# Optimization experiments

Measured on AMD Instinct MI355X. Metric: run time of the kernel, lower is better.

Reference implementation:

```python
import jax, jax.numpy as jnp
import numpy as np

HIDDEN = 1024
HEADS = 16
HEAD_DIM = HIDDEN // HEADS


def setup_inputs() -> dict:
    key = jax.random.key(0)
    ks = jax.random.split(key, 9)
    B, S, D = 8, 1370, HIDDEN
    x = jax.random.normal(ks[0], (B, S, D), dtype=jnp.float32)
    s = 1.0 / np.sqrt(D)
    Wq = jax.random.normal(ks[1], (D, D), dtype=jnp.float32) * s
    bq = jnp.zeros((D,), dtype=jnp.float32)
    Wk = jax.random.normal(ks[2], (D, D), dtype=jnp.float32) * s
    bk = jnp.zeros((D,), dtype=jnp.float32)
    Wv = jax.random.normal(ks[3], (D, D), dtype=jnp.float32) * s
    bv = jnp.zeros((D,), dtype=jnp.float32)
    Wo = jax.random.normal(ks[4], (D, D), dtype=jnp.float32) * s
    bo = jnp.zeros((D,), dtype=jnp.float32)
    return {"x": x, "Wq": Wq, "bq": bq, "Wk": Wk, "bk": bk,
            "Wv": Wv, "bv": bv, "Wo": Wo, "bo": bo}


def reference(x, Wq, bq, Wk, bk, Wv, bv, Wo, bo):
    B, S, D = x.shape
    H, Dh = HEADS, HEAD_DIM
    # separate Q/K/V projections
    q = (x @ Wq + bq).reshape(B, S, H, Dh).transpose(0, 2, 1, 3)  # [B,H,S,Dh]
    k = (x @ Wk + bk).reshape(B, S, H, Dh).transpose(0, 2, 1, 3)
    v = (x @ Wv + bv).reshape(B, S, H, Dh).transpose(0, 2, 1, 3)
    scale = jnp.asarray(Dh, q.dtype) ** -0.5
    attn = jnp.einsum('bhqd,bhkd->bhqk', q, k) * scale  # [B,H,S,S]
    attn = jax.nn.softmax(attn, axis=-1)
    out = jnp.einsum('bhqk,bhkd->bhqd', attn, v)        # [B,H,S,Dh]
    out = out.transpose(0, 2, 1, 3).reshape(B, S, D)
    return out @ Wo + bo
```

## Files before the change

kernel.cpp:

```cpp
#include <hip/hip_runtime.h>
#include <stdint.h>

#define DEV __device__ __forceinline__

typedef unsigned short u16;
typedef __attribute__((ext_vector_type(8))) __bf16 bf16x8;
typedef __attribute__((ext_vector_type(8))) u16 u16x8;
typedef __attribute__((ext_vector_type(4))) u16 u16x4;
typedef __attribute__((ext_vector_type(4))) float floatx4;

#define S_LEN 1370
#define S_PAD 1408
#define NH 16
#define DH 64
#define M_TOK (8 * S_LEN)
#define NKT (S_PAD / 64)

DEV u16 f2bf(float f) {
    union { float f; uint32_t u; } v; v.f = f;
    uint32_t u = v.u + 0x7fffu + ((v.u >> 16) & 1u);
    return (u16)(u >> 16);
}

typedef const __attribute__((address_space(1))) void as1_cvoid;
typedef __attribute__((address_space(3))) void as3_void;

DEV void async16(const void* g, void* s) {
    __builtin_amdgcn_global_load_lds((as1_cvoid*)g, (as3_void*)s, 16, 0, 0);
}

__global__ void cvt_bf16(const float* __restrict__ src, u16* __restrict__ dst) {
    const size_t i0 = ((size_t)blockIdx.x * 256 + threadIdx.x) * 8;
    const float4 a = *(const float4*)(src + i0);
    const float4 b = *(const float4*)(src + i0 + 4);
    u16x8 o;
    o[0] = f2bf(a.x); o[1] = f2bf(a.y); o[2] = f2bf(a.z); o[3] = f2bf(a.w);
    o[4] = f2bf(b.x); o[5] = f2bf(b.y); o[6] = f2bf(b.z); o[7] = f2bf(b.w);
    *(u16x8*)(dst + i0) = o;
}

__global__ void transpose4(const float* __restrict__ w0, const float* __restrict__ w1,
                           const float* __restrict__ w2, const float* __restrict__ w3,
                           u16* __restrict__ t0, u16* __restrict__ t1,
                           u16* __restrict__ t2, u16* __restrict__ t3) {
    __shared__ u16 tile[64][65];
    const float* src; u16* dst;
    switch (blockIdx.z) {
        case 0: src = w0; dst = t0; break;
        case 1: src = w1; dst = t1; break;
        case 2: src = w2; dst = t2; break;
        default: src = w3; dst = t3; break;
    }
    const int tx = blockIdx.x, ty = blockIdx.y, tid = threadIdx.x;
#pragma unroll
    for (int i = 0; i < 16; i++) {
        int e = i * 256 + tid, r = e >> 6, c = e & 63;
        tile[r][c] = f2bf(src[(size_t)(ty * 64 + r) * 1024 + tx * 64 + c]);
    }
    __syncthreads();
#pragma unroll
    for (int i = 0; i < 16; i++) {
        int e = i * 256 + tid, r = e >> 6, c = e & 63;
        dst[(size_t)(tx * 64 + r) * 1024 + ty * 64 + c] = tile[c][r];
    }
}

template <int MODE>
__global__ void gemm_bt(const u16* __restrict__ A, const u16* __restrict__ BT,
                        const float* __restrict__ bias, void* __restrict__ Cv,
                        int M, int N) {
    __shared__ u16 As[128 * 32];
    __shared__ u16 Bs[128 * 32];
    const int tid = threadIdx.x;
    const int w = tid >> 6, lane = tid & 63, quad = lane >> 4, l15 = lane & 15;
    const int mbase = blockIdx.x * 128, nbase = blockIdx.y * 128;
    const int wm = (w >> 1) * 64, wn = (w & 1) * 64;

    floatx4 acc[4][4];
#pragma unroll
    for (int i = 0; i < 4; i++)
#pragma unroll
        for (int j = 0; j < 4; j++) acc[i][j] = (floatx4){0.f, 0.f, 0.f, 0.f};

    const int srow = tid >> 2;
    const int kb = (tid & 3) * 16;
    int ar0 = mbase + srow;          if (ar0 > M - 1) ar0 = M - 1;
    int ar1 = mbase + 64 + srow;     if (ar1 > M - 1) ar1 = M - 1;
    int br0 = nbase + srow;          if (br0 > N - 1) br0 = N - 1;
    int br1 = nbase + 64 + srow;     if (br1 > N - 1) br1 = N - 1;
    const char* pA = (const char*)A;
    const char* pB = (const char*)BT;
    char* ldsA = (char*)As + w * 1024;
    char* ldsB = (char*)Bs + w * 1024;

    for (int kt = 0; kt < 32; kt++) {
        const int koff = kt * 64 + kb;
        async16(pA + (size_t)ar0 * 2048 + koff, ldsA);
        async16(pA + (size_t)ar1 * 2048 + koff, ldsA + 4096);
        async16(pB + (size_t)br0 * 2048 + koff, ldsB);
        async16(pB + (size_t)br1 * 2048 + koff, ldsB + 4096);
        __syncthreads();
        bf16x8 af[4], bfv[4];
#pragma unroll
        for (int mi = 0; mi < 4; mi++)
            af[mi] = __builtin_bit_cast(bf16x8,
                *(const u16x8*)&As[(wm + mi * 16 + l15) * 32 + quad * 8]);
#pragma unroll
        for (int ni = 0; ni < 4; ni++)
            bfv[ni] = __builtin_bit_cast(bf16x8,
                *(const u16x8*)&Bs[(wn + ni * 16 + l15) * 32 + quad * 8]);
#pragma unroll
        for (int mi = 0; mi < 4; mi++)
#pragma unroll
            for (int ni = 0; ni < 4; ni++)
                acc[mi][ni] = __builtin_amdgcn_mfma_f32_16x16x32_bf16(
                    af[mi], bfv[ni], acc[mi][ni], 0, 0, 0);
        __syncthreads();
    }

    if (MODE == 0 || MODE == 2) {
#pragma unroll
        for (int ni = 0; ni < 4; ni++) {
            const int n = nbase + wn + ni * 16 + l15;
            const float bv = bias[n];
#pragma unroll
            for (int mi = 0; mi < 4; mi++)
#pragma unroll
                for (int r = 0; r < 4; r++) {
                    const int m = mbase + wm + mi * 16 + quad * 4 + r;
                    if (m < M) {
                        if (MODE == 0)
                            ((u16*)Cv)[(size_t)m * 1024 + n] = f2bf(acc[mi][ni][r] + bv);
                        else
                            ((float*)Cv)[(size_t)m * 1024 + n] = acc[mi][ni][r] + bv;
                    }
                }
        }
    } else {
        u16* C = (u16*)Cv;
#pragma unroll
        for (int mi = 0; mi < 4; mi++)
#pragma unroll
            for (int r = 0; r < 4; r++) {
                const int mf = mbase + wm + mi * 16 + quad * 4 + r;
                const int h = mf >> 6, d = mf & 63;
                const float bv = bias[mf];
#pragma unroll
                for (int ni = 0; ni < 4; ni++) {
                    const int t = nbase + wn + ni * 16 + l15;
                    if (t < N) {
                        const int b = t / S_LEN;
                        const int s = t - b * S_LEN;
                        C[(size_t)((b * NH + h) * DH + d) * S_PAD + s] =
                            f2bf(acc[mi][ni][r] + bv);
                    }
                }
            }
    }
}

__global__ void flash_attn(const u16* __restrict__ Q, const u16* __restrict__ K,
                           const u16* __restrict__ VT, u16* __restrict__ O) {
    __shared__ u16 Ks[2 * 64 * 32];
    __shared__ u16 Vs[2 * 64 * 32];
    __shared__ u16 Ps[2][32 * 72];

    const int tid = threadIdx.x;
    const int w = tid >> 6, lane = tid & 63, quad = lane >> 4, l15 = lane & 15;
    const int qt = blockIdx.x, bh = blockIdx.y, b = bh >> 4, h = bh & 15;
    const int q0 = qt * 64 + w * 32;

    bf16x8 qf[2][2];
#pragma unroll
    for (int mi = 0; mi < 2; mi++) {
        int qr = q0 + mi * 16 + l15;
        if (qr > S_LEN - 1) qr = S_LEN - 1;
        const u16* qp = Q + (size_t)(b * S_LEN + qr) * 1024 + h * 64 + quad * 8;
        qf[mi][0] = __builtin_bit_cast(bf16x8, *(const u16x8*)qp);
        qf[mi][1] = __builtin_bit_cast(bf16x8, *(const u16x8*)(qp + 32));
    }

    floatx4 o_acc[2][4];
#pragma unroll
    for (int mi = 0; mi < 2; mi++)
#pragma unroll
        for (int nd = 0; nd < 4; nd++) o_acc[mi][nd] = (floatx4){0.f, 0.f, 0.f, 0.f};
    float mrun[2] = {-1e30f, -1e30f}, lrun[2] = {0.f, 0.f};

    const int scol = ((lane & 3) ^ ((lane >> 3) & 3)) * 16;
    const int lrow = lane >> 2;
    const char* Kbl = (const char*)K + ((size_t)b * S_LEN * 1024 + h * 64) * 2 + scol;
    const char* Vbl = (const char*)VT +
                      ((size_t)(bh * 64 + w * 32 + lrow) * S_PAD) * 2 + scol;
    char* KsB = (char*)Ks;
    char* VsB = (char*)Vs;
    u16* Pw = Ps[w];

    const int rcol = ((quad ^ ((l15 >> 1) & 3)) * 16);

    const float CEXP = 0.18033688f;

    for (int kt = 0; kt < NKT; kt++) {
#pragma unroll
        for (int i = 0; i < 2; i++) {
            const int r0 = w * 32 + i * 16;
            int key = kt * 64 + r0 + lrow;
            if (key > S_LEN - 1) key = S_LEN - 1;
            const char* kg = Kbl + (size_t)key * 2048;
            async16(kg, KsB + r0 * 64);
            async16(kg + 64, KsB + 4096 + r0 * 64);
            const char* vg = Vbl + (size_t)i * (16 * S_PAD * 2) + kt * 128;
            async16(vg, VsB + r0 * 64);
            async16(vg + 64, VsB + 4096 + r0 * 64);
        }
        __syncthreads();

        floatx4 st[2][4];
#pragma unroll
        for (int mi = 0; mi < 2; mi++)
#pragma unroll
            for (int ni = 0; ni < 4; ni++) st[mi][ni] = (floatx4){0.f, 0.f, 0.f, 0.f};
#pragma unroll
        for (int kk = 0; kk < 2; kk++)
#pragma unroll
            for (int ni = 0; ni < 4; ni++) {
                bf16x8 kf = __builtin_bit_cast(bf16x8,
                    *(const u16x8*)(KsB + kk * 4096 + (ni * 16 + l15) * 64 + rcol));
                st[0][ni] = __builtin_amdgcn_mfma_f32_16x16x32_bf16(kf, qf[0][kk], st[0][ni], 0, 0, 0);
                st[1][ni] = __builtin_amdgcn_mfma_f32_16x16x32_bf16(kf, qf[1][kk], st[1][ni], 0, 0, 0);
            }

        if (kt == NKT - 1) {
#pragma unroll
            for (int ni = 0; ni < 4; ni++)
#pragma unroll
                for (int r = 0; r < 4; r++) {
                    const bool oob = (kt * 64 + ni * 16 + quad * 4 + r) >= S_LEN;
                    if (oob) { st[0][ni][r] = -1e30f; st[1][ni][r] = -1e30f; }
                }
        }

        float alphav[2];
#pragma unroll
        for (int mi = 0; mi < 2; mi++) {
            float mx = -1e30f;
#pragma unroll
            for (int ni = 0; ni < 4; ni++)
#pragma unroll
                for (int r = 0; r < 4; r++) mx = fmaxf(mx, st[mi][ni][r]);
            mx = fmaxf(mx, __shfl_xor(mx, 16));
            mx = fmaxf(mx, __shfl_xor(mx, 32));
            const float mnew = fmaxf(mrun[mi], mx);
            alphav[mi] = __builtin_amdgcn_exp2f((mrun[mi] - mnew) * CEXP);
            mrun[mi] = mnew;
            float rs = 0.f;
#pragma unroll
            for (int ni = 0; ni < 4; ni++) {
                u16x4 pq;
#pragma unroll
                for (int r = 0; r < 4; r++) {
                    const float p = __builtin_amdgcn_exp2f((st[mi][ni][r] - mnew) * CEXP);
                    rs += p;
                    union { float f; uint32_t u; } cv; cv.f = p;
                    pq[r] = (u16)((cv.u + 0x8000u) >> 16);
                }
                *(u16x4*)&Pw[(mi * 16 + l15) * 72 + ni * 16 + quad * 4] = pq;
            }
            rs += __shfl_xor(rs, 16);
            rs += __shfl_xor(rs, 32);
            lrun[mi] = lrun[mi] * alphav[mi] + rs;
        }

#pragma unroll
        for (int mi = 0; mi < 2; mi++)
#pragma unroll
            for (int r = 0; r < 4; r++) {
                const float a = __shfl(alphav[mi], quad * 4 + r);
#pragma unroll
                for (int nd = 0; nd < 4; nd++) o_acc[mi][nd][r] *= a;
            }

        __asm__ __volatile__("" ::: "memory");

#pragma unroll
        for (int kk = 0; kk < 2; kk++) {
            bf16x8 pf0 = __builtin_bit_cast(bf16x8,
                *(const u16x8*)&Pw[(l15) * 72 + kk * 32 + quad * 8]);
            bf16x8 pf1 = __builtin_bit_cast(bf16x8,
                *(const u16x8*)&Pw[(16 + l15) * 72 + kk * 32 + quad * 8]);
#pragma unroll
            for (int nd = 0; nd < 4; nd++) {
                bf16x8 vf = __builtin_bit_cast(bf16x8,
                    *(const u16x8*)(VsB + kk * 4096 + (nd * 16 + l15) * 64 + rcol));
                o_acc[0][nd] = __builtin_amdgcn_mfma_f32_16x16x32_bf16(pf0, vf, o_acc[0][nd], 0, 0, 0);
                o_acc[1][nd] = __builtin_amdgcn_mfma_f32_16x16x32_bf16(pf1, vf, o_acc[1][nd], 0, 0, 0);
            }
        }
        __syncthreads();
    }

    const float linv0 = 1.f / lrun[0], linv1 = 1.f / lrun[1];
#pragma unroll
    for (int mi = 0; mi < 2; mi++)
#pragma unroll
        for (int r = 0; r < 4; r++) {
            const float inv = __shfl(mi == 0 ? linv0 : linv1, quad * 4 + r);
            const int q = q0 + mi * 16 + quad * 4 + r;
            if (q < S_LEN) {
                u16* op = O + (size_t)(b * S_LEN + q) * 1024 + h * 64;
#pragma unroll
                for (int nd = 0; nd < 4; nd++)
                    op[nd * 16 + l15] = f2bf(o_acc[mi][nd][r] * inv);
            }
        }
}

extern "C" void kernel_launch(void* const* d_in, const int* in_sizes, int n_in,
                              void* d_out, int out_size, void* d_ws, size_t ws_size,
                              hipStream_t stream) {
    const float* x  = (const float*)d_in[0];
    const float* Wq = (const float*)d_in[1];
    const float* bq = (const float*)d_in[2];
    const float* Wk = (const float*)d_in[3];
    const float* bk = (const float*)d_in[4];
    const float* Wv = (const float*)d_in[5];
    const float* bv = (const float*)d_in[6];
    const float* Wo = (const float*)d_in[7];
    const float* bo = (const float*)d_in[8];
    float* out = (float*)d_out;

    u16* WqT = (u16*)d_ws;
    u16* WkT = WqT + (size_t)1024 * 1024;
    u16* WvT = WkT + (size_t)1024 * 1024;
    u16* WoT = WvT + (size_t)1024 * 1024;
    u16* xb  = WoT + (size_t)1024 * 1024;
    u16* Qb  = xb + (size_t)M_TOK * 1024;
    u16* Kb  = Qb + (size_t)M_TOK * 1024;
    u16* VTb = Kb + (size_t)M_TOK * 1024;
    u16* Ob  = VTb + (size_t)128 * 64 * S_PAD;

    cvt_bf16<<<dim3(M_TOK * 1024 / 2048), 256, 0, stream>>>(x, xb);
    transpose4<<<dim3(16, 16, 4), 256, 0, stream>>>(Wq, Wk, Wv, Wo, WqT, WkT, WvT, WoT);
    gemm_bt<0><<<dim3(86, 8), 256, 0, stream>>>(xb, WqT, bq, Qb, M_TOK, 1024);
    gemm_bt<0><<<dim3(86, 8), 256, 0, stream>>>(xb, WkT, bk, Kb, M_TOK, 1024);
    gemm_bt<1><<<dim3(8, 86), 256, 0, stream>>>(WvT, xb, bv, VTb, 1024, M_TOK);
    flash_attn<<<dim3(22, 128), 128, 0, stream>>>(Qb, Kb, VTb, Ob);
    gemm_bt<2><<<dim3(86, 8), 256, 0, stream>>>(Ob, WoT, bo, out, M_TOK, 1024);
}
```

Before: 426.0 us.

## Fuse Q/K projections into one GEMM and double-buffer flash attention tiles

Q and K projections now run as a single GEMM over the concatenated WqT/WkT, which relies on the two weights being contiguous in the workspace. Each block routes its output to Q or K by column range, saving one launch and improving wave fill. Flash attention now uses 4 waves per block covering 128 queries, so K/V tiles are shared across more queries. It double-buffers K/V in LDS, prefetching the next tile while computing the current one, at the cost of more LDS and possible occupancy loss.

```diff
diff --git a/kernel.cpp b/kernel.cpp
--- a/kernel.cpp
+++ b/kernel.cpp
@@ -65,6 +65,77 @@
     }
 }
 
+#define GEMM_KLOOP(M_, N_)                                                     \
+    floatx4 acc[4][4];                                                         \
+    _Pragma("unroll")                                                          \
+    for (int i = 0; i < 4; i++)                                                \
+        _Pragma("unroll")                                                      \
+        for (int j = 0; j < 4; j++) acc[i][j] = (floatx4){0.f, 0.f, 0.f, 0.f}; \
+    const int srow = tid >> 2;                                                 \
+    const int kb = (tid & 3) * 16;                                             \
+    int ar0 = mbase + srow;          if (ar0 > (M_) - 1) ar0 = (M_) - 1;       \
+    int ar1 = mbase + 64 + srow;     if (ar1 > (M_) - 1) ar1 = (M_) - 1;       \
+    int br0 = nbase + srow;          if (br0 > (N_) - 1) br0 = (N_) - 1;       \
+    int br1 = nbase + 64 + srow;     if (br1 > (N_) - 1) br1 = (N_) - 1;       \
+    const char* pA = (const char*)A;                                           \
+    const char* pB = (const char*)BT;                                          \
+    char* ldsA = (char*)As + w * 1024;                                         \
+    char* ldsB = (char*)Bs + w * 1024;                                         \
+    for (int kt = 0; kt < 32; kt++) {                                          \
+        const int koff = kt * 64 + kb;                                         \
+        async16(pA + (size_t)ar0 * 2048 + koff, ldsA);                         \
+        async16(pA + (size_t)ar1 * 2048 + koff, ldsA + 4096);                  \
+        async16(pB + (size_t)br0 * 2048 + koff, ldsB);                         \
+        async16(pB + (size_t)br1 * 2048 + koff, ldsB + 4096);                  \
+        __syncthreads();                                                       \
+        bf16x8 af[4], bfv[4];                                                  \
+        _Pragma("unroll")                                                      \
+        for (int mi = 0; mi < 4; mi++)                                         \
+            af[mi] = __builtin_bit_cast(bf16x8,                                \
+                *(const u16x8*)&As[(wm + mi * 16 + l15) * 32 + quad * 8]);     \
+        _Pragma("unroll")                                                      \
+        for (int ni = 0; ni < 4; ni++)                                         \
+            bfv[ni] = __builtin_bit_cast(bf16x8,                               \
+                *(const u16x8*)&Bs[(wn + ni * 16 + l15) * 32 + quad * 8]);     \
+        _Pragma("unroll")                                                      \
+        for (int mi = 0; mi < 4; mi++)                                         \
+            _Pragma("unroll")                                                  \
+            for (int ni = 0; ni < 4; ni++)                                     \
+                acc[mi][ni] = __builtin_amdgcn_mfma_f32_16x16x32_bf16(         \
+                    af[mi], bfv[ni], acc[mi][ni], 0, 0, 0);                    \
+        __syncthreads();                                                       \
+    }
+
+__global__ void gemm_qk(const u16* __restrict__ A, const u16* __restrict__ BT,
+                        const float* __restrict__ bq, const float* __restrict__ bk,
+                        u16* __restrict__ Cq, u16* __restrict__ Ck, int M) {
+    __shared__ u16 As[128 * 32];
+    __shared__ u16 Bs[128 * 32];
+    const int tid = threadIdx.x;
+    const int w = tid >> 6, lane = tid & 63, quad = lane >> 4, l15 = lane & 15;
+    const int mbase = blockIdx.x * 128, nbase = blockIdx.y * 128;
+    const int wm = (w >> 1) * 64, wn = (w & 1) * 64;
+
+    GEMM_KLOOP(M, 2048)
+
+    const bool isQ = nbase < 1024;
+    u16* C = isQ ? Cq : Ck;
+    const float* bias = isQ ? bq : bk;
+    const int nb = (isQ ? nbase : nbase - 1024) + wn;
+#pragma unroll
+    for (int ni = 0; ni < 4; ni++) {
+        const int n = nb + ni * 16 + l15;
+        const float bv = bias[n];
+#pragma unroll
+        for (int mi = 0; mi < 4; mi++)
+#pragma unroll
+            for (int r = 0; r < 4; r++) {
+                const int m = mbase + wm + mi * 16 + quad * 4 + r;
+                if (m < M) C[(size_t)m * 1024 + n] = f2bf(acc[mi][ni][r] + bv);
+            }
+    }
+}
+
 template <int MODE>
 __global__ void gemm_bt(const u16* __restrict__ A, const u16* __restrict__ BT,
                         const float* __restrict__ bias, void* __restrict__ Cv,
@@ -76,49 +147,9 @@
     const int mbase = blockIdx.x * 128, nbase = blockIdx.y * 128;
     const int wm = (w >> 1) * 64, wn = (w & 1) * 64;
 
-    floatx4 acc[4][4];
-#pragma unroll
-    for (int i = 0; i < 4; i++)
-#pragma unroll
-        for (int j = 0; j < 4; j++) acc[i][j] = (floatx4){0.f, 0.f, 0.f, 0.f};
-
-    const int srow = tid >> 2;
-    const int kb = (tid & 3) * 16;
-    int ar0 = mbase + srow;          if (ar0 > M - 1) ar0 = M - 1;
-    int ar1 = mbase + 64 + srow;     if (ar1 > M - 1) ar1 = M - 1;
-    int br0 = nbase + srow;          if (br0 > N - 1) br0 = N - 1;
-    int br1 = nbase + 64 + srow;     if (br1 > N - 1) br1 = N - 1;
-    const char* pA = (const char*)A;
-    const char* pB = (const char*)BT;
-    char* ldsA = (char*)As + w * 1024;
-    char* ldsB = (char*)Bs + w * 1024;
-
-    for (int kt = 0; kt < 32; kt++) {
-        const int koff = kt * 64 + kb;
-        async16(pA + (size_t)ar0 * 2048 + koff, ldsA);
-        async16(pA + (size_t)ar1 * 2048 + koff, ldsA + 4096);
-        async16(pB + (size_t)br0 * 2048 + koff, ldsB);
-        async16(pB + (size_t)br1 * 2048 + koff, ldsB + 4096);
-        __syncthreads();
-        bf16x8 af[4], bfv[4];
-#pragma unroll
-        for (int mi = 0; mi < 4; mi++)
-            af[mi] = __builtin_bit_cast(bf16x8,
-                *(const u16x8*)&As[(wm + mi * 16 + l15) * 32 + quad * 8]);
-#pragma unroll
-        for (int ni = 0; ni < 4; ni++)
-            bfv[ni] = __builtin_bit_cast(bf16x8,
-                *(const u16x8*)&Bs[(wn + ni * 16 + l15) * 32 + quad * 8]);
-#pragma unroll
-        for (int mi = 0; mi < 4; mi++)
-#pragma unroll
-            for (int ni = 0; ni < 4; ni++)
-                acc[mi][ni] = __builtin_amdgcn_mfma_f32_16x16x32_bf16(
-                    af[mi], bfv[ni], acc[mi][ni], 0, 0, 0);
-        __syncthreads();
-    }
-
-    if (MODE == 0 || MODE == 2) {
+    GEMM_KLOOP(M, N)
+
+    if (MODE == 2) {
 #pragma unroll
         for (int ni = 0; ni < 4; ni++) {
             const int n = nbase + wn + ni * 16 + l15;
@@ -128,12 +159,7 @@
 #pragma unroll
                 for (int r = 0; r < 4; r++) {
                     const int m = mbase + wm + mi * 16 + quad * 4 + r;
-                    if (m < M) {
-                        if (MODE == 0)
-                            ((u16*)Cv)[(size_t)m * 1024 + n] = f2bf(acc[mi][ni][r] + bv);
-                        else
-                            ((float*)Cv)[(size_t)m * 1024 + n] = acc[mi][ni][r] + bv;
-                    }
+                    if (m < M) ((float*)Cv)[(size_t)m * 1024 + n] = acc[mi][ni][r] + bv;
                 }
         }
     } else {
@@ -161,14 +187,14 @@
 
 __global__ void flash_attn(const u16* __restrict__ Q, const u16* __restrict__ K,
                            const u16* __restrict__ VT, u16* __restrict__ O) {
-    __shared__ u16 Ks[2 * 64 * 32];
-    __shared__ u16 Vs[2 * 64 * 32];
-    __shared__ u16 Ps[2][32 * 72];
+    __shared__ u16 Ks[2][2 * 64 * 32];
+    __shared__ u16 Vs[2][2 * 64 * 32];
+    __shared__ u16 Ps[4][32 * 72];
 
     const int tid = threadIdx.x;
     const int w = tid >> 6, lane = tid & 63, quad = lane >> 4, l15 = lane & 15;
-    const int qt = blockIdx.x, bh = blockIdx.y, b = bh >> 4, h = bh & 15;
-    const int q0 = qt * 64 + w * 32;
+    const int bh = blockIdx.x, b = bh >> 4, h = bh & 15;
+    const int q0 = blockIdx.y * 128 + w * 32;
 
     bf16x8 qf[2][2];
 #pragma unroll
@@ -187,33 +213,41 @@
         for (int nd = 0; nd < 4; nd++) o_acc[mi][nd] = (floatx4){0.f, 0.f, 0.f, 0.f};
     float mrun[2] = {-1e30f, -1e30f}, lrun[2] = {0.f, 0.f};
 
+    const int lrow = lane >> 2;
     const int scol = ((lane & 3) ^ ((lane >> 3) & 3)) * 16;
-    const int lrow = lane >> 2;
     const char* Kbl = (const char*)K + ((size_t)b * S_LEN * 1024 + h * 64) * 2 + scol;
     const char* Vbl = (const char*)VT +
-                      ((size_t)(bh * 64 + w * 32 + lrow) * S_PAD) * 2 + scol;
+                      ((size_t)(bh * 64 + w * 16 + lrow) * S_PAD) * 2 + scol;
     char* KsB = (char*)Ks;
     char* VsB = (char*)Vs;
     u16* Pw = Ps[w];
 
-    const int rcol = ((quad ^ ((l15 >> 1) & 3)) * 16);
+    const int rcol = (quad ^ ((l15 >> 1) & 3)) * 16;
 
     const float CEXP = 0.18033688f;
 
+#define STAGE(KT, BI)                                                          \
+    {                                                                          \
+        int key_ = (KT) * 64 + w * 16 + lrow;                                  \
+        if (key_ > S_LEN - 1) key_ = S_LEN - 1;                                \
+        const char* kg_ = Kbl + (size_t)key_ * 2048;                           \
+        char* kd_ = KsB + (BI) * 8192 + (w * 16) * 64;                         \
+        async16(kg_, kd_);                                                     \
+        async16(kg_ + 64, kd_ + 4096);                                         \
+        const char* vg_ = Vbl + (KT) * 128;                                    \
+        char* vd_ = VsB + (BI) * 8192 + (w * 16) * 64;                         \
+        async16(vg_, vd_);                                                     \
+        async16(vg_ + 64, vd_ + 4096);                                         \
+    }
+
+    STAGE(0, 0)
+    __syncthreads();
+
     for (int kt = 0; kt < NKT; kt++) {
-#pragma unroll
-        for (int i = 0; i < 2; i++) {
-            const int r0 = w * 32 + i * 16;
-            int key = kt * 64 + r0 + lrow;
-            if (key > S_LEN - 1) key = S_LEN - 1;
-            const char* kg = Kbl + (size_t)key * 2048;
-            async16(kg, KsB + r0 * 64);
-            async16(kg + 64, KsB + 4096 + r0 * 64);
-            const char* vg = Vbl + (size_t)i * (16 * S_PAD * 2) + kt * 128;
-            async16(vg, VsB + r0 * 64);
-            async16(vg + 64, VsB + 4096 + r0 * 64);
-        }
-        __syncthreads();
+        const int bi = kt & 1;
+        if (kt + 1 < NKT) STAGE(kt + 1, bi ^ 1)
+        const char* KsT = KsB + bi * 8192;
+        const char* VsT = VsB + bi * 8192;
 
         floatx4 st[2][4];
 #pragma unroll
@@ -225,7 +259,7 @@
 #pragma unroll
             for (int ni = 0; ni < 4; ni++) {
                 bf16x8 kf = __builtin_bit_cast(bf16x8,
-                    *(const u16x8*)(KsB + kk * 4096 + (ni * 16 + l15) * 64 + rcol));
+                    *(const u16x8*)(KsT + kk * 4096 + (ni * 16 + l15) * 64 + rcol));
                 st[0][ni] = __builtin_amdgcn_mfma_f32_16x16x32_bf16(kf, qf[0][kk], st[0][ni], 0, 0, 0);
                 st[1][ni] = __builtin_amdgcn_mfma_f32_16x16x32_bf16(kf, qf[1][kk], st[1][ni], 0, 0, 0);
             }
@@ -291,7 +325,7 @@
 #pragma unroll
             for (int nd = 0; nd < 4; nd++) {
                 bf16x8 vf = __builtin_bit_cast(bf16x8,
-                    *(const u16x8*)(VsB + kk * 4096 + (nd * 16 + l15) * 64 + rcol));
+                    *(const u16x8*)(VsT + kk * 4096 + (nd * 16 + l15) * 64 + rcol));
                 o_acc[0][nd] = __builtin_amdgcn_mfma_f32_16x16x32_bf16(pf0, vf, o_acc[0][nd], 0, 0, 0);
                 o_acc[1][nd] = __builtin_amdgcn_mfma_f32_16x16x32_bf16(pf1, vf, o_acc[1][nd], 0, 0, 0);
             }
@@ -341,9 +375,8 @@
 
     cvt_bf16<<<dim3(M_TOK * 1024 / 2048), 256, 0, stream>>>(x, xb);
     transpose4<<<dim3(16, 16, 4), 256, 0, stream>>>(Wq, Wk, Wv, Wo, WqT, WkT, WvT, WoT);
-    gemm_bt<0><<<dim3(86, 8), 256, 0, stream>>>(xb, WqT, bq, Qb, M_TOK, 1024);
-    gemm_bt<0><<<dim3(86, 8), 256, 0, stream>>>(xb, WkT, bk, Kb, M_TOK, 1024);
+    gemm_qk<<<dim3(86, 16), 256, 0, stream>>>(xb, WqT, bq, bk, Qb, Kb, M_TOK);
     gemm_bt<1><<<dim3(8, 86), 256, 0, stream>>>(WvT, xb, bv, VTb, 1024, M_TOK);
-    flash_attn<<<dim3(22, 128), 128, 0, stream>>>(Qb, Kb, VTb, Ob);
+    flash_attn<<<dim3(128, 11), 256, 0, stream>>>(Qb, Kb, VTb, Ob);
     gemm_bt<2><<<dim3(86, 8), 256, 0, stream>>>(Ob, WoT, bo, out, M_TOK, 1024);
 }
```

Result: faster. 404.3 us (-5.1%).
